# Performance work log

Measured on AMD Instinct MI355X. Metric: run time of the kernel, lower is better.

## Reference

```python
import jax, jax.numpy as jnp
import numpy as np

B, H, E, G, SEQ_LEN = 131072, 64, 16, 32, 30


def setup_inputs() -> dict:
    key = jax.random.key(0)
    ks = jax.random.split(key, 17)
    def lin(kw, kb, out_f, in_f):
        s = 1.0 / np.sqrt(in_f)
        W = jax.random.uniform(kw, (out_f, in_f), jnp.float32, -s, s)
        b = jax.random.uniform(kb, (out_f,), jnp.float32, -s, s)
        return W, b
    W_se, b_se = lin(ks[0], ks[1], E, 2)
    W_h2p, b_h2p = lin(ks[2], ks[3], 2, 3 * H)
    W_goal, b_goal = lin(ks[4], ks[5], H, 2 * G)
    W_abs, b_abs = lin(ks[6], ks[7], H, 2)
    W_ih, b_ih = lin(ks[8], ks[9], 4 * H, E)
    W_hh, b_hh = lin(ks[10], ks[11], 4 * H, H)
    return {
        "traj_abs": jax.random.normal(ks[12], (1, B, 2), jnp.float32),
        "traj_rel": jax.random.normal(ks[13], (1, B, 2), jnp.float32),
        "h0": jax.random.normal(ks[14], (1, B, H), jnp.float32),
        "c0": jax.random.normal(ks[15], (1, B, H), jnp.float32),
        "goals": jax.random.normal(ks[16], (B, G, 2), jnp.float32),
        "W_ih": W_ih, "W_hh": W_hh, "b_ih": b_ih, "b_hh": b_hh,
        "W_se": W_se, "b_se": b_se,
        "W_h2p": W_h2p, "b_h2p": b_h2p,
        "W_goal": W_goal, "b_goal": b_goal,
        "W_abs": W_abs, "b_abs": b_abs,
    }


def reference(traj_abs, traj_rel, h0, c0, goals,
              W_ih, W_hh, b_ih, b_hh,
              W_se, b_se, W_h2p, b_h2p,
              W_goal, b_goal, W_abs, b_abs):
    b = traj_abs.shape[1]
    goal_emb = goals.reshape(b, -1) @ W_goal.T + b_goal            # (b, H)
    dec_in = jax.nn.leaky_relu(traj_rel[0] @ W_se.T + b_se)        # (b, E)

    def step(carry, _):
        h, c, x, abs_pos = carry
        gates = x @ W_ih.T + b_ih + h @ W_hh.T + b_hh              # (b, 4H)
        i, f, g, o = jnp.split(gates, 4, axis=-1)                  # PyTorch gate order
        c = jax.nn.sigmoid(f) * c + jax.nn.sigmoid(i) * jnp.tanh(g)
        h = jax.nn.sigmoid(o) * jnp.tanh(c)
        abs_emb = abs_pos @ W_abs.T + b_abs                        # (b, H)
        inp = jnp.concatenate([h, abs_emb, goal_emb], axis=1)      # (b, 3H)
        rel = inp @ W_h2p.T + b_h2p                                # (b, 2)
        x = jax.nn.leaky_relu(rel @ W_se.T + b_se)
        return (h, c, x, abs_pos + rel), rel

    _, rels = jax.lax.scan(step, (h0[0], c0[0], dec_in, traj_abs[0]),
                           None, length=SEQ_LEN)
    return rels  # (seq_len, b, 2)
```

## Files before the change

kernel.cpp:

```cpp
#include <hip/hip_runtime.h>
#include <stdint.h>


#define B_TOT 131072
#define SEQL 30

typedef _Float16 f16x8 __attribute__((ext_vector_type(8)));
typedef _Float16 f16x2 __attribute__((ext_vector_type(2)));
typedef float f32x4 __attribute__((ext_vector_type(4)));
typedef float f32x2 __attribute__((ext_vector_type(2)));

__device__ __forceinline__ float fexp2(float x) {
#if __has_builtin(__builtin_amdgcn_exp2f)
  return __builtin_amdgcn_exp2f(x);
#else
  return exp2f(x);
#endif
}
__device__ __forceinline__ float frcp(float x) {
#if __has_builtin(__builtin_amdgcn_rcpf)
  return __builtin_amdgcn_rcpf(x);
#else
  return 1.0f / x;
#endif
}

__global__ void setup_consts(const float* __restrict__ Wgoal,
                             const float* __restrict__ bgoal,
                             const float* __restrict__ Wh2p,
                             const float* __restrict__ bh2p,
                             const float* __restrict__ Wabs,
                             const float* __restrict__ babs,
                             float* __restrict__ wsf) {
  const int tid = threadIdx.x;
  const int wv = tid >> 6;
  const int lane = tid & 63;
  if (wv == 0) {
    const int k = lane;
    float s0 = 0.f, s1 = 0.f;
#pragma unroll 8
    for (int jj = 0; jj < 64; ++jj) {
      float wg = Wgoal[jj * 64 + k];
      s0 += wg * Wh2p[128 + jj];
      s1 += wg * Wh2p[320 + jj];
    }
    wsf[k] = s0;
    wsf[64 + k] = s1;
  } else {
    const int i = lane >> 3, sub = lane & 7;
    const int p = i & 1, grp = i >> 1;
    float s = 0.f;
#pragma unroll
    for (int t = 0; t < 8; ++t) {
      int j = sub * 8 + t;
      float wv_ = (grp < 3) ? Wh2p[p * 192 + 64 + j] : Wh2p[p * 192 + 128 + j];
      float av = (grp == 0)   ? Wabs[j * 2 + 0]
                 : (grp == 1) ? Wabs[j * 2 + 1]
                 : (grp == 2) ? babs[j]
                              : bgoal[j];
      s += av * wv_;
    }
    s += __shfl_xor(s, 1, 64);
    s += __shfl_xor(s, 2, 64);
    s += __shfl_xor(s, 4, 64);
    if (sub == 0) {
      if (grp == 2) s += bh2p[p];
      wsf[128 + i] = s;
    }
  }
}

__global__ __launch_bounds__(256, 3) void lstm_mfma(
    const float* __restrict__ tabs, const float* __restrict__ trel,
    const float* __restrict__ h0, const float* __restrict__ c0,
    const float* __restrict__ goals, const float* __restrict__ Wih,
    const float* __restrict__ Whh, const float* __restrict__ bih,
    const float* __restrict__ bhh, const float* __restrict__ Wse,
    const float* __restrict__ bse, const float* __restrict__ Wh2p,
    const float* __restrict__ wsf, float* __restrict__ outp) {
  const int lane = threadIdx.x & 63;
  const int w = threadIdx.x >> 6;
  const int q = lane >> 4;
  const int n = lane & 15;
  const int pm = n & 3;
  const int hs = 16 * w;
  const int bbase = blockIdx.x * 16;

  __shared__ __align__(16) _Float16 hbuf[2 * 16 * 72];

  const float SI = -1.4426950408889634f;
  const float SG = 2.8853900817779268f;
  const float gsc[4] = {SI, SI, SG, SI};
  f16x8 bw[4][3];
#pragma unroll
  for (int g = 0; g < 4; ++g) {
    const int row = g * 64 + hs + n;
    const float sc = gsc[g];
#pragma unroll
    for (int kk = 0; kk < 2; ++kk)
#pragma unroll
      for (int j = 0; j < 8; ++j)
        bw[g][kk][j] = (_Float16)(sc * Whh[row * 64 + kk * 32 + q * 8 + j]);
    float bfold = 0.f, m20 = 0.f, m21 = 0.f;
#pragma unroll
    for (int k = 0; k < 16; ++k) {
      float wik = Wih[row * 16 + k];
      bfold += bse[k] * wik;
      m20 += Wse[k * 2 + 0] * wik;
      m21 += Wse[k * 2 + 1] * wik;
    }
    float bias = sc * (bih[row] + bhh[row] + 0.505f * bfold);
#pragma unroll
    for (int j = 0; j < 8; ++j) {
      float v;
      if (q < 2)
        v = sc * Wih[row * 16 + q * 8 + j];
      else if (q == 2 && j == 0)
        v = bias;
      else if (q == 2 && j == 1)
        v = sc * 0.505f * m20;
      else if (q == 2 && j == 2)
        v = sc * 0.505f * m21;
      else
        v = 0.f;
      bw[g][2][j] = (_Float16)v;
    }
  }
  f16x8 awp0, awp1;
#pragma unroll
  for (int j = 0; j < 8; ++j) {
    float v0 = (pm < 2) ? Wh2p[pm * 192 + q * 8 + j] : 0.f;
    float v1 = (pm < 2) ? Wh2p[pm * 192 + 32 + q * 8 + j] : 0.f;
    awp0[j] = (_Float16)v0;
    awp1[j] = (_Float16)v1;
  }
  const float Sx0 = wsf[128], Sx1 = wsf[129];
  const float Sy0 = wsf[130], Sy1 = wsf[131];

  f16x2 wsaP[4], wsbP[4], bscP[4];
  const uint32_t xmask = (q < 2) ? 0x7FFF7FFFu : 0xFFFFFFFFu;
#pragma unroll
  for (int jj = 0; jj < 4; ++jj) {
    f16x2 z = f16x2{(_Float16)0.f, (_Float16)0.f};
    if (q < 2) {
      int kx = q * 8 + 2 * jj;
      wsaP[jj] =
          f16x2{(_Float16)(0.495f * Wse[kx * 2 + 0]),
                (_Float16)(0.495f * Wse[kx * 2 + 2])};
      wsbP[jj] =
          f16x2{(_Float16)(0.495f * Wse[kx * 2 + 1]),
                (_Float16)(0.495f * Wse[kx * 2 + 3])};
      bscP[jj] = f16x2{(_Float16)(0.495f * bse[kx]),
                       (_Float16)(0.495f * bse[kx + 1])};
    } else if (q == 2 && jj == 0) {
      wsaP[jj] = f16x2{(_Float16)0.f, (_Float16)1.f};
      wsbP[jj] = z;
      bscP[jj] = f16x2{(_Float16)1.f, (_Float16)0.f};
    } else if (q == 2 && jj == 1) {
      wsaP[jj] = z;
      wsbP[jj] = f16x2{(_Float16)1.f, (_Float16)0.f};
      bscP[jj] = z;
    } else {
      wsaP[jj] = z;
      wsbP[jj] = z;
      bscP[jj] = z;
    }
  }

  auto build_x = [&](float r0f, float r1f) -> f16x8 {
    f16x2 r0h = f16x2{(_Float16)r0f, (_Float16)r0f};
    f16x2 r1h = f16x2{(_Float16)r1f, (_Float16)r1f};
    f16x8 xr;
#pragma unroll
    for (int jj = 0; jj < 4; ++jj) {
      f16x2 t = r0h * wsaP[jj] + (r1h * wsbP[jj] + bscP[jj]);
      uint32_t tu = __builtin_bit_cast(uint32_t, t) & xmask;
      f16x2 lr = __builtin_bit_cast(f16x2, tu);
      xr[2 * jj] = lr[0];
      xr[2 * jj + 1] = lr[1];
    }
    return xr;
  };

  const f32x4 zC = {0.f, 0.f, 0.f, 0.f};
  f32x4 GaccT;
  {
    f16x8 aM0, aM1, bg0, bg1;
#pragma unroll
    for (int j = 0; j < 8; ++j) {
      int k = q * 8 + j;
      aM0[j] = (_Float16)((pm < 2) ? wsf[pm * 64 + k] : 0.f);
      aM1[j] = (_Float16)((pm < 2) ? wsf[pm * 64 + 32 + k] : 0.f);
      bg0[j] = (_Float16)goals[(bbase + n) * 64 + k];
      bg1[j] = (_Float16)goals[(bbase + n) * 64 + 32 + k];
    }
    GaccT = __builtin_amdgcn_mfma_f32_16x16x32_f16(aM0, bg0, zC, 0, 0, 0);
    GaccT = __builtin_amdgcn_mfma_f32_16x16x32_f16(aM1, bg1, GaccT, 0, 0, 0);
    GaccT[0] += wsf[132] + wsf[134];
    GaccT[1] += wsf[133] + wsf[135];
  }

  float ax = tabs[(bbase + n) * 2 + 0];
  float ay = tabs[(bbase + n) * 2 + 1];
  float cst[4];
#pragma unroll
  for (int r = 0; r < 4; ++r) {
    const int b = bbase + 4 * q + r;
    cst[r] = c0[b * 64 + hs + n];
    hbuf[(4 * q + r) * 72 + hs + n] = (_Float16)h0[b * 64 + hs + n];
  }

  f16x8 xf = build_x(trel[(bbase + n) * 2 + 0], trel[(bbase + n) * 2 + 1]);

  const int ro = n * 72 + q * 8;
  const int wo = (4 * q) * 72 + hs + n;
  const float K2 = 2.8853900817779268f;

  int poff = 0;
  for (int s = 0; s <= SEQL; ++s) {
    __syncthreads();
    const f16x8 ah0 = *(const f16x8*)(hbuf + poff + ro);
    const f16x8 ah1 = *(const f16x8*)(hbuf + poff + ro + 32);

    if (s > 0) {
      f32x4 pa =
          __builtin_amdgcn_mfma_f32_16x16x32_f16(awp0, ah0, GaccT, 0, 0, 0);
      pa = __builtin_amdgcn_mfma_f32_16x16x32_f16(awp1, ah1, pa, 0, 0, 0);
      float u0 = pa[0] + fmaf(ax, Sx0, ay * Sy0);
      float u1 = pa[1] + fmaf(ax, Sx1, ay * Sy1);
      ax += u0;
      ay += u1;
      if (w == 0 && lane < 16) {
        float2 v;
        v.x = u0;
        v.y = u1;
        ((float2*)outp)[(size_t)(s - 1) * B_TOT + bbase + lane] = v;
      }
      xf = build_x(u0, u1);
    }

    if (s < SEQL) {
      f32x4 acc[4];
#pragma unroll
      for (int g = 0; g < 4; ++g) {
        f32x4 a = __builtin_amdgcn_mfma_f32_16x16x32_f16(ah0, bw[g][0], zC,
                                                         0, 0, 0);
        a = __builtin_amdgcn_mfma_f32_16x16x32_f16(ah1, bw[g][1], a, 0, 0, 0);
        a = __builtin_amdgcn_mfma_f32_16x16x32_f16(xf, bw[g][2], a, 0, 0, 0);
        acc[g] = a;
      }
      _Float16* hw = hbuf + (poff ^ 1152) + wo;
#pragma unroll
      for (int pr = 0; pr < 2; ++pr) {
        const int ra = 2 * pr, rb = 2 * pr + 1;
        f32x2 Av = {fexp2(acc[0][ra]), fexp2(acc[0][rb])};
        f32x2 Fv = {fexp2(acc[1][ra]), fexp2(acc[1][rb])};
        f32x2 Bv = {fexp2(acc[2][ra]), fexp2(acc[2][rb])};
        const f32x2 one = {1.f, 1.f};
        f32x2 t1 = Av + one;
        f32x2 t2 = Bv + one;
        f32x2 t3 = Fv + one;
        f32x2 t4 = Bv - one;
        f32x2 m1 = t1 * t2;
        f32x2 cs = {cst[ra], cst[rb]};
        f32x2 num = cs * m1 + t4 * t3;
        f32x2 den = m1 * t3;
        f32x2 cc = {num[0] * frcp(den[0]), num[1] * frcp(den[1])};
        cst[ra] = cc[0];
        cst[rb] = cc[1];
        f32x2 Cv = {fexp2(acc[3][ra]), fexp2(acc[3][rb])};
        f32x2 k2c = cc * K2;
        f32x2 Dv = {fexp2(k2c[0]), fexp2(k2c[1])};
        f32x2 hd = (Cv + one) * (Dv + one);
        f32x2 hnm = Dv - one;
        hw[72 * ra] = (_Float16)(hnm[0] * frcp(hd[0]));
        hw[72 * rb] = (_Float16)(hnm[1] * frcp(hd[1]));
      }
      poff ^= 1152;
    }
  }
}

extern "C" void kernel_launch(void* const* d_in, const int* in_sizes, int n_in,
                              void* d_out, int out_size, void* d_ws,
                              size_t ws_size, hipStream_t stream) {
  (void)in_sizes; (void)n_in; (void)out_size; (void)ws_size;
  const float* tabs  = (const float*)d_in[0];
  const float* trel  = (const float*)d_in[1];
  const float* h0    = (const float*)d_in[2];
  const float* c0    = (const float*)d_in[3];
  const float* goals = (const float*)d_in[4];
  const float* Wih   = (const float*)d_in[5];
  const float* Whh   = (const float*)d_in[6];
  const float* bih   = (const float*)d_in[7];
  const float* bhh   = (const float*)d_in[8];
  const float* Wse   = (const float*)d_in[9];
  const float* bse   = (const float*)d_in[10];
  const float* Wh2p  = (const float*)d_in[11];
  const float* bh2p  = (const float*)d_in[12];
  const float* Wgoal = (const float*)d_in[13];
  const float* bgoal = (const float*)d_in[14];
  const float* Wabs  = (const float*)d_in[15];
  const float* babs  = (const float*)d_in[16];
  float* wsf = (float*)d_ws;

  setup_consts<<<dim3(1), dim3(128), 0, stream>>>(Wgoal, bgoal, Wh2p, bh2p,
                                                  Wabs, babs, wsf);
  lstm_mfma<<<dim3(8192), dim3(256), 0, stream>>>(
      tabs, trel, h0, c0, goals, Wih, Whh, bih, bhh, Wse, bse, Wh2p, wsf,
      (float*)d_out);
}
```

Measured before the change: 539.5 us.

## Process two 16-row batch tiles per block to amortize weight registers and barriers

Each block now handles two 16-sample batch tiles with the same register-resident W_hh/W_ih fragments. The MFMA chains of the two tiles are interleaved, and the per-step barrier, setup and weight loads are shared across both tiles. The grid is halved and launch bounds are raised to 4 blocks per CU. This adds register pressure from the doubled accumulators and state, which could cause spills or lower occupancy.

```diff
diff --git a/kernel.cpp b/kernel.cpp
--- a/kernel.cpp
+++ b/kernel.cpp
@@ -4,6 +4,7 @@
 
 #define B_TOT 131072
 #define SEQL 30
+#define NT 2
 
 typedef _Float16 f16x8 __attribute__((ext_vector_type(8)));
 typedef _Float16 f16x2 __attribute__((ext_vector_type(2)));
@@ -70,7 +71,7 @@
   }
 }
 
-__global__ __launch_bounds__(256, 3) void lstm_mfma(
+__global__ __launch_bounds__(256, 4) void lstm_mfma(
     const float* __restrict__ tabs, const float* __restrict__ trel,
     const float* __restrict__ h0, const float* __restrict__ c0,
     const float* __restrict__ goals, const float* __restrict__ Wih,
@@ -84,9 +85,9 @@
   const int n = lane & 15;
   const int pm = n & 3;
   const int hs = 16 * w;
-  const int bbase = blockIdx.x * 16;
-
-  __shared__ __align__(16) _Float16 hbuf[2 * 16 * 72];
+  const int bbase = blockIdx.x * (16 * NT);
+
+  __shared__ __align__(16) _Float16 hbuf[2 * NT * 16 * 72];
 
   const float SI = -1.4426950408889634f;
   const float SG = 2.8853900817779268f;
@@ -183,34 +184,48 @@
   };
 
   const f32x4 zC = {0.f, 0.f, 0.f, 0.f};
-  f32x4 GaccT;
+
+  f32x4 GaccT[NT];
+  float ax[NT], ay[NT], cst[NT][4];
+  f16x8 xf[NT];
   {
-    f16x8 aM0, aM1, bg0, bg1;
+    f16x8 aM0, aM1;
 #pragma unroll
     for (int j = 0; j < 8; ++j) {
       int k = q * 8 + j;
       aM0[j] = (_Float16)((pm < 2) ? wsf[pm * 64 + k] : 0.f);
       aM1[j] = (_Float16)((pm < 2) ? wsf[pm * 64 + 32 + k] : 0.f);
-      bg0[j] = (_Float16)goals[(bbase + n) * 64 + k];
-      bg1[j] = (_Float16)goals[(bbase + n) * 64 + 32 + k];
-    }
-    GaccT = __builtin_amdgcn_mfma_f32_16x16x32_f16(aM0, bg0, zC, 0, 0, 0);
-    GaccT = __builtin_amdgcn_mfma_f32_16x16x32_f16(aM1, bg1, GaccT, 0, 0, 0);
-    GaccT[0] += wsf[132] + wsf[134];
-    GaccT[1] += wsf[133] + wsf[135];
-  }
-
-  float ax = tabs[(bbase + n) * 2 + 0];
-  float ay = tabs[(bbase + n) * 2 + 1];
-  float cst[4];
-#pragma unroll
-  for (int r = 0; r < 4; ++r) {
-    const int b = bbase + 4 * q + r;
-    cst[r] = c0[b * 64 + hs + n];
-    hbuf[(4 * q + r) * 72 + hs + n] = (_Float16)h0[b * 64 + hs + n];
-  }
-
-  f16x8 xf = build_x(trel[(bbase + n) * 2 + 0], trel[(bbase + n) * 2 + 1]);
+    }
+    const float Sb0 = wsf[132] + wsf[134];
+    const float Sb1 = wsf[133] + wsf[135];
+#pragma unroll
+    for (int t = 0; t < NT; ++t) {
+      const int bb = bbase + 16 * t;
+      f16x8 bg0, bg1;
+#pragma unroll
+      for (int j = 0; j < 8; ++j) {
+        int k = q * 8 + j;
+        bg0[j] = (_Float16)goals[(bb + n) * 64 + k];
+        bg1[j] = (_Float16)goals[(bb + n) * 64 + 32 + k];
+      }
+      f32x4 Ga = __builtin_amdgcn_mfma_f32_16x16x32_f16(aM0, bg0, zC, 0, 0, 0);
+      Ga = __builtin_amdgcn_mfma_f32_16x16x32_f16(aM1, bg1, Ga, 0, 0, 0);
+      Ga[0] += Sb0;
+      Ga[1] += Sb1;
+      GaccT[t] = Ga;
+
+      ax[t] = tabs[(bb + n) * 2 + 0];
+      ay[t] = tabs[(bb + n) * 2 + 1];
+#pragma unroll
+      for (int r = 0; r < 4; ++r) {
+        const int b = bb + 4 * q + r;
+        cst[t][r] = c0[b * 64 + hs + n];
+        hbuf[t * 1152 + (4 * q + r) * 72 + hs + n] =
+            (_Float16)h0[b * 64 + hs + n];
+      }
+      xf[t] = build_x(trel[(bb + n) * 2 + 0], trel[(bb + n) * 2 + 1]);
+    }
+  }
 
   const int ro = n * 72 + q * 8;
   const int wo = (4 * q) * 72 + hs + n;
@@ -219,64 +234,83 @@
   int poff = 0;
   for (int s = 0; s <= SEQL; ++s) {
     __syncthreads();
-    const f16x8 ah0 = *(const f16x8*)(hbuf + poff + ro);
-    const f16x8 ah1 = *(const f16x8*)(hbuf + poff + ro + 32);
+    f16x8 ah0[NT], ah1[NT];
+#pragma unroll
+    for (int t = 0; t < NT; ++t) {
+      ah0[t] = *(const f16x8*)(hbuf + poff + t * 1152 + ro);
+      ah1[t] = *(const f16x8*)(hbuf + poff + t * 1152 + ro + 32);
+    }
 
     if (s > 0) {
-      f32x4 pa =
-          __builtin_amdgcn_mfma_f32_16x16x32_f16(awp0, ah0, GaccT, 0, 0, 0);
-      pa = __builtin_amdgcn_mfma_f32_16x16x32_f16(awp1, ah1, pa, 0, 0, 0);
-      float u0 = pa[0] + fmaf(ax, Sx0, ay * Sy0);
-      float u1 = pa[1] + fmaf(ax, Sx1, ay * Sy1);
-      ax += u0;
-      ay += u1;
-      if (w == 0 && lane < 16) {
-        float2 v;
-        v.x = u0;
-        v.y = u1;
-        ((float2*)outp)[(size_t)(s - 1) * B_TOT + bbase + lane] = v;
-      }
-      xf = build_x(u0, u1);
+      f32x4 pa[NT];
+#pragma unroll
+      for (int t = 0; t < NT; ++t) {
+        f32x4 p = __builtin_amdgcn_mfma_f32_16x16x32_f16(awp0, ah0[t],
+                                                         GaccT[t], 0, 0, 0);
+        pa[t] = __builtin_amdgcn_mfma_f32_16x16x32_f16(awp1, ah1[t], p,
+                                                       0, 0, 0);
+      }
+#pragma unroll
+      for (int t = 0; t < NT; ++t) {
+        float u0 = pa[t][0] + fmaf(ax[t], Sx0, ay[t] * Sy0);
+        float u1 = pa[t][1] + fmaf(ax[t], Sx1, ay[t] * Sy1);
+        ax[t] += u0;
+        ay[t] += u1;
+        if (w == t && lane < 16) {
+          float2 v;
+          v.x = u0;
+          v.y = u1;
+          ((float2*)outp)[(size_t)(s - 1) * B_TOT + bbase + 16 * t + lane] = v;
+        }
+        xf[t] = build_x(u0, u1);
+      }
     }
 
     if (s < SEQL) {
-      f32x4 acc[4];
-#pragma unroll
-      for (int g = 0; g < 4; ++g) {
-        f32x4 a = __builtin_amdgcn_mfma_f32_16x16x32_f16(ah0, bw[g][0], zC,
-                                                         0, 0, 0);
-        a = __builtin_amdgcn_mfma_f32_16x16x32_f16(ah1, bw[g][1], a, 0, 0, 0);
-        a = __builtin_amdgcn_mfma_f32_16x16x32_f16(xf, bw[g][2], a, 0, 0, 0);
-        acc[g] = a;
-      }
-      _Float16* hw = hbuf + (poff ^ 1152) + wo;
-#pragma unroll
-      for (int pr = 0; pr < 2; ++pr) {
-        const int ra = 2 * pr, rb = 2 * pr + 1;
-        f32x2 Av = {fexp2(acc[0][ra]), fexp2(acc[0][rb])};
-        f32x2 Fv = {fexp2(acc[1][ra]), fexp2(acc[1][rb])};
-        f32x2 Bv = {fexp2(acc[2][ra]), fexp2(acc[2][rb])};
-        const f32x2 one = {1.f, 1.f};
-        f32x2 t1 = Av + one;
-        f32x2 t2 = Bv + one;
-        f32x2 t3 = Fv + one;
-        f32x2 t4 = Bv - one;
-        f32x2 m1 = t1 * t2;
-        f32x2 cs = {cst[ra], cst[rb]};
-        f32x2 num = cs * m1 + t4 * t3;
-        f32x2 den = m1 * t3;
-        f32x2 cc = {num[0] * frcp(den[0]), num[1] * frcp(den[1])};
-        cst[ra] = cc[0];
-        cst[rb] = cc[1];
-        f32x2 Cv = {fexp2(acc[3][ra]), fexp2(acc[3][rb])};
-        f32x2 k2c = cc * K2;
-        f32x2 Dv = {fexp2(k2c[0]), fexp2(k2c[1])};
-        f32x2 hd = (Cv + one) * (Dv + one);
-        f32x2 hnm = Dv - one;
-        hw[72 * ra] = (_Float16)(hnm[0] * frcp(hd[0]));
-        hw[72 * rb] = (_Float16)(hnm[1] * frcp(hd[1]));
-      }
-      poff ^= 1152;
+      f32x4 acc[NT][4];
+#pragma unroll
+      for (int g = 0; g < 4; ++g)
+#pragma unroll
+        for (int t = 0; t < NT; ++t) {
+          f32x4 a = __builtin_amdgcn_mfma_f32_16x16x32_f16(ah0[t], bw[g][0],
+                                                           zC, 0, 0, 0);
+          a = __builtin_amdgcn_mfma_f32_16x16x32_f16(ah1[t], bw[g][1], a,
+                                                     0, 0, 0);
+          a = __builtin_amdgcn_mfma_f32_16x16x32_f16(xf[t], bw[g][2], a,
+                                                     0, 0, 0);
+          acc[t][g] = a;
+        }
+#pragma unroll
+      for (int t = 0; t < NT; ++t) {
+        _Float16* hw = hbuf + (poff ^ 2304) + t * 1152 + wo;
+#pragma unroll
+        for (int pr = 0; pr < 2; ++pr) {
+          const int ra = 2 * pr, rb = 2 * pr + 1;
+          f32x2 Av = {fexp2(acc[t][0][ra]), fexp2(acc[t][0][rb])};
+          f32x2 Fv = {fexp2(acc[t][1][ra]), fexp2(acc[t][1][rb])};
+          f32x2 Bv = {fexp2(acc[t][2][ra]), fexp2(acc[t][2][rb])};
+          const f32x2 one = {1.f, 1.f};
+          f32x2 t1 = Av + one;
+          f32x2 t2 = Bv + one;
+          f32x2 t3 = Fv + one;
+          f32x2 t4 = Bv - one;
+          f32x2 m1 = t1 * t2;
+          f32x2 cs = {cst[t][ra], cst[t][rb]};
+          f32x2 num = cs * m1 + t4 * t3;
+          f32x2 den = m1 * t3;
+          f32x2 cc = {num[0] * frcp(den[0]), num[1] * frcp(den[1])};
+          cst[t][ra] = cc[0];
+          cst[t][rb] = cc[1];
+          f32x2 Cv = {fexp2(acc[t][3][ra]), fexp2(acc[t][3][rb])};
+          f32x2 k2c = cc * K2;
+          f32x2 Dv = {fexp2(k2c[0]), fexp2(k2c[1])};
+          f32x2 hd = (Cv + one) * (Dv + one);
+          f32x2 hnm = Dv - one;
+          hw[72 * ra] = (_Float16)(hnm[0] * frcp(hd[0]));
+          hw[72 * rb] = (_Float16)(hnm[1] * frcp(hd[1]));
+        }
+      }
+      poff ^= 2304;
     }
   }
 }
@@ -306,7 +340,7 @@
 
   setup_consts<<<dim3(1), dim3(128), 0, stream>>>(Wgoal, bgoal, Wh2p, bh2p,
                                                   Wabs, babs, wsf);
-  lstm_mfma<<<dim3(8192), dim3(256), 0, stream>>>(
+  lstm_mfma<<<dim3(B_TOT / (16 * NT)), dim3(256), 0, stream>>>(
       tabs, trel, h0, c0, goals, Wih, Whh, bih, bhh, Wse, bse, Wh2p, wsf,
       (float*)d_out);
 }
```

After: 562.9 us. +4.3%, slower.
